# Performance work log

Measured on AMD Instinct MI355X. Metric: run time of the kernel, lower is better.

The kernel has to match this reference:

```python
import jax, jax.numpy as jnp
import numpy as np

N, C = 2, 256
GH0, GW0 = 40, 40
GH1, GW1 = 40, 40
STRIDE, TOPK = 2, 8
TEMP, THRESH, BORDER = 0.1, 0.2, 2
H0, W0 = GH0 * STRIDE, GW0 * STRIDE
H1, W1 = GH1 * STRIDE, GW1 * STRIDE
K4 = TOPK * STRIDE * STRIDE
# create_meshgrid(2,2) flattened: entries (x, y) in row-major (y outer) order
GRID = jnp.array([[0, 0], [1, 0], [0, 1], [1, 1]], dtype=jnp.int32)


def map_indices(idx, size0, size1):
    # idx: (n, G0, topk) coarse indices into image1 coarse grid
    row = idx[..., None] // size1[1] * STRIDE + GRID[:, 1]
    col = idx[..., None] % size1[1] * STRIDE + GRID[:, 0]
    fine = row * (size1[1] * STRIDE) + col  # (n, G0, topk, 4)
    n = idx.shape[0]
    fine = fine.reshape(n, size0[0], 1, size0[1], 1, -1)
    fine = jnp.broadcast_to(fine, (n, size0[0], STRIDE, size0[1], STRIDE, fine.shape[-1]))
    return fine.reshape(n, size0[0] * size0[1] * STRIDE * STRIDE, -1)


def remove_border_one_side(idx, br, size):
    h, w = size
    pos = jnp.arange(h * w)
    r, c = pos // w, pos % w
    border = (r < br) | (r >= h - br) | (c < br) | (c >= w - br)
    return jnp.where(border[None, :], 0, idx)


def unpatchify(x, grid, stride):
    n, g, s2, c = x.shape
    gh, gw = grid
    x = x.reshape(n, gh, gw, stride, stride, c)
    x = jnp.transpose(x, (0, 5, 1, 3, 2, 4))
    return x.reshape(n, c, gh * stride, gw * stride)


def fused_heatmaps(x0, x1, a01, a10, ind0_f, ind1_f):
    s01 = jnp.einsum('ngqc,ngkc->ngqk', x0, a01) / C  # (n, G0, 4, K4)
    s10 = jnp.einsum('ngqc,ngkc->ngqk', x1, a10) / C
    h01 = jax.nn.softmax(s01 / TEMP, axis=-1)
    h10 = jax.nn.softmax(s10 / TEMP, axis=-1)
    h01 = h01.reshape(N, GH0, GW0, STRIDE, STRIDE, K4)
    h01 = jnp.transpose(h01, (0, 1, 3, 2, 4, 5)).reshape(N, H0 * W0, K4)
    h10 = h10.reshape(N, GH1, GW1, STRIDE, STRIDE, K4)
    h10 = jnp.transpose(h10, (0, 5, 1, 3, 2, 4)).reshape(N, K4, H1 * W1)
    # dense scatter + gather mutual fusion (as in the torch code)
    b = jnp.arange(N)[:, None, None]
    l1 = jnp.arange(H1 * W1)[None, None, :]
    Z0 = jnp.zeros((N, H0 * W0, H1 * W1), h10.dtype).at[b, ind1_f, l1].set(h10)
    new_h01 = h01 * jnp.take_along_axis(Z0, ind0_f, axis=-1)
    l0 = jnp.arange(H0 * W0)[None, :, None]
    Z1 = jnp.zeros((N, H0 * W0, H1 * W1), h01.dtype).at[b, l0, ind0_f].set(h01)
    new_h10 = h10 * jnp.take_along_axis(Z1, ind1_f, axis=-2)
    return new_h01, new_h10


def coarse_matching(h01, h10, ind0_f, ind1_f):
    score = jnp.max(h01, axis=-1)                 # (n, L0)
    sub0 = jnp.argmax(h01, axis=-1)               # (n, L0)
    j_best = jnp.take_along_axis(ind0_f, sub0[..., None], axis=-1)[..., 0]
    sub1 = jnp.argmax(h10, axis=-2)               # (n, L1)
    i_best = jnp.take_along_axis(ind1_f, sub1[:, None, :], axis=-2)[:, 0, :]
    j_best = remove_border_one_side(j_best, BORDER, (H1, W1))
    i_best = remove_border_one_side(i_best, BORDER, (H0, W0))
    biproj = jnp.take_along_axis(i_best, j_best, axis=-1)
    mask = biproj == jnp.arange(H0 * W0)[None, :]
    mask = mask.at[:, 0].set(False)
    mask = mask & (score > THRESH)
    scores = jnp.where(mask, score, 0.0)
    return mask, j_best, scores


def setup_inputs() -> dict:
    key = jax.random.key(0)
    ks = jax.random.split(key, 6)
    return {
        'x0': jax.random.normal(ks[0], (N, GH0 * GW0, 4, C), jnp.float32),
        'x1': jax.random.normal(ks[1], (N, GH1 * GW1, 4, C), jnp.float32),
        'attended0_to_1': jax.random.normal(ks[2], (N, GH0 * GW0, K4, C), jnp.float32),
        'attended1_to_0': jax.random.normal(ks[3], (N, GH1 * GW1, K4, C), jnp.float32),
        'x0_prior': jax.random.normal(ks[4], (N, C, GH0, GW0), jnp.float32),
        'x1_prior': jax.random.normal(ks[5], (N, C, GH1, GW1), jnp.float32),
    }


def reference(x0, x1, attended0_to_1, attended1_to_0, x0_prior, x1_prior):
    p0 = x0_prior.reshape(N, C, GH0 * GW0)
    p1 = x1_prior.reshape(N, C, GH1 * GW1)
    sim = jnp.einsum('nci,ncj->nij', p0, p1) / C  # (n, G0, G1)
    _, i01 = jax.lax.top_k(sim, TOPK)                              # (n, G0, topk)
    _, i10 = jax.lax.top_k(jnp.swapaxes(sim, -2, -1), TOPK)        # (n, G1, topk)
    ind0_f = map_indices(i01, (GH0, GW0), (GH1, GW1))              # (n, L0, K4)
    ind1_f = jnp.swapaxes(map_indices(i10, (GH1, GW1), (GH0, GW0)), -2, -1)  # (n, K4, L1)
    h01, h10 = fused_heatmaps(x0, x1, attended0_to_1, attended1_to_0, ind0_f, ind1_f)
    mask, j_best, scores = coarse_matching(jax.lax.stop_gradient(h01), jax.lax.stop_gradient(h10), ind0_f, ind1_f)
    x0_8x = unpatchify(x0, (GH0, GW0), STRIDE)
    x1_8x = unpatchify(x1, (GH1, GW1), STRIDE)
    return h01, h10, scores, j_best, mask, x0_8x, x1_8x
```

## Files before the change

### kernel.cpp

```cpp
#include <hip/hip_runtime.h>


#define N_B   2
#define C_DIM 256
#define G0N   1600
#define GW    40
#define L0N   6400
#define W_F   80
#define TK    8

#define KC 32
#define HEAT_N   6400
#define SIM_BASE 6400
#define SIM_N    1250
#define UNP_BASE 7650
#define UNP_N    7680
#define MEGA_N   15330

__global__ __launch_bounds__(256) void k_mega(
    const float* __restrict__ x0,  const float* __restrict__ a01, float* __restrict__ h01p,
    const float* __restrict__ x1,  const float* __restrict__ a10, float* __restrict__ h10p,
    const float* __restrict__ p0,  const float* __restrict__ p1,
    float* __restrict__ sim, float* __restrict__ simT,
    float* __restrict__ out0, float* __restrict__ out1) {
  __shared__ __align__(16) float lds[4096];
  const int bid = blockIdx.x;
  const int t   = threadIdx.x;

  if (bid < HEAT_N) {
    const float* x   = x0;
    const float* att = a01;
    float*      hpre = h01p;
    int ng = bid;
    if (bid >= N_B * G0N) { x = x1; att = a10; hpre = h10p; ng = bid - N_B * G0N; }
    float* xs = lds;
    float (*dots)[33] = (float(*)[33])(lds + 1024);

    *(float4*)&xs[t * 4] = *(const float4*)(x + (size_t)ng * 4 * C_DIM + t * 4);

    const int row = t >> 3;
    const int sub = t & 7;
    const float* ar = att + ((size_t)ng * 32 + row) * C_DIM + sub * 4;
    float4 av[8];
#pragma unroll
    for (int it = 0; it < 8; ++it) av[it] = *(const float4*)(ar + it * 32);

    __syncthreads();

    float a0 = 0.f, a1 = 0.f, a2 = 0.f, a3 = 0.f;
#pragma unroll
    for (int it = 0; it < 8; ++it) {
      const int xo = sub * 4 + it * 32;
      float4 xv0 = *(const float4*)&xs[0 * C_DIM + xo];
      float4 xv1 = *(const float4*)&xs[1 * C_DIM + xo];
      float4 xv2 = *(const float4*)&xs[2 * C_DIM + xo];
      float4 xv3 = *(const float4*)&xs[3 * C_DIM + xo];
      a0 += av[it].x * xv0.x + av[it].y * xv0.y + av[it].z * xv0.z + av[it].w * xv0.w;
      a1 += av[it].x * xv1.x + av[it].y * xv1.y + av[it].z * xv1.z + av[it].w * xv1.w;
      a2 += av[it].x * xv2.x + av[it].y * xv2.y + av[it].z * xv2.z + av[it].w * xv2.w;
      a3 += av[it].x * xv3.x + av[it].y * xv3.y + av[it].z * xv3.z + av[it].w * xv3.w;
    }
#pragma unroll
    for (int off = 1; off < 8; off <<= 1) {
      a0 += __shfl_xor(a0, off);
      a1 += __shfl_xor(a1, off);
      a2 += __shfl_xor(a2, off);
      a3 += __shfl_xor(a3, off);
    }
    if (sub == 0) {
      dots[0][row] = a0;
      dots[1][row] = a1;
      dots[2][row] = a2;
      dots[3][row] = a3;
    }
    __syncthreads();
    if (t < 128) {
      int q = t >> 5, k4 = t & 31;
      float l = (dots[q][k4] * (1.0f / 256.0f)) / 0.1f;
      float m = l;
#pragma unroll
      for (int off = 1; off < 32; off <<= 1) m = fmaxf(m, __shfl_xor(m, off));
      float e = expf(l - m);
      float s = e;
#pragma unroll
      for (int off = 1; off < 32; off <<= 1) s += __shfl_xor(s, off);
      hpre[(size_t)ng * 128 + q * 32 + k4] = e / s;
    }
  } else if (bid < UNP_BASE) {
    int s = bid - SIM_BASE;
    const int n  = s / 625; s -= n * 625;
    const int i0 = (s / 25) * 64;
    const int j0 = (s % 25) * 64;
    const float* A = p0 + (size_t)n * C_DIM * G0N;
    const float* B = p1 + (size_t)n * C_DIM * G0N;
    float* As = lds;
    float* Bs = lds + 2048;
    const int tx = t & 15;
    const int ty = t >> 4;

    float4 acc[4];
#pragma unroll
    for (int ii = 0; ii < 4; ++ii) acc[ii] = make_float4(0.f, 0.f, 0.f, 0.f);

    for (int kc = 0; kc < C_DIM; kc += KC) {
#pragma unroll
      for (int u = 0; u < 2; ++u) {
        int f   = t + u * 256;
        int row = f >> 4;
        int c4  = (f & 15) * 4;
        *(float4*)&As[row * 64 + c4] = *(const float4*)(A + (size_t)(kc + row) * G0N + i0 + c4);
        *(float4*)&Bs[row * 64 + c4] = *(const float4*)(B + (size_t)(kc + row) * G0N + j0 + c4);
      }
      __syncthreads();
#pragma unroll
      for (int k = 0; k < KC; ++k) {
        __attribute__((aligned(16))) float a[4];
        *(float4*)&a[0] = *(const float4*)&As[k * 64 + ty * 4];
        float4 bv = *(const float4*)&Bs[k * 64 + tx * 4];
#pragma unroll
        for (int ii = 0; ii < 4; ++ii) {
          acc[ii].x += a[ii] * bv.x;
          acc[ii].y += a[ii] * bv.y;
          acc[ii].z += a[ii] * bv.z;
          acc[ii].w += a[ii] * bv.w;
        }
      }
      __syncthreads();
    }

    float* simn  = sim  + (size_t)n * G0N * G0N;
    float* simTn = simT + (size_t)n * G0N * G0N;
    const int ib = i0 + ty * 4;
    const int jb = j0 + tx * 4;
    const float* accf = (const float*)acc;
#pragma unroll
    for (int ii = 0; ii < 4; ++ii)
      *(float4*)(simn + (size_t)(ib + ii) * G0N + jb) = acc[ii];
#pragma unroll
    for (int jj = 0; jj < 4; ++jj) {
      float4 col = make_float4(accf[0 * 4 + jj], accf[1 * 4 + jj],
                               accf[2 * 4 + jj], accf[3 * 4 + jj]);
      *(float4*)(simTn + (size_t)(jb + jj) * G0N + ib) = col;
    }
  } else {
    int u = bid - UNP_BASE;
    int ux = u % 3; u /= 3;
    int r  = u % 80; u /= 80;
    int z  = u;
    const float* x = (z < 16) ? x0 : x1;
    float* out     = (z < 16) ? out0 : out1;
    int zz  = z & 15;
    int cc0 = ux * 32;
    int n   = zz >> 3;
    int c0  = (zz & 7) * 32;
    float (*tile)[33] = (float(*)[33])lds;
    int sr = r & 1, ghr = r >> 1;
    int pos = t >> 5, cl = t & 31;
#pragma unroll
    for (int it = 0; it < 4; ++it) {
      int p = pos + it * 8;
      int cc = cc0 + p;
      if (cc < W_F) {
        int gg = ghr * GW + (cc >> 1);
        int qq = (sr << 1) | (cc & 1);
        tile[p][cl] = x[(((size_t)n * G0N + gg) * 4 + qq) * C_DIM + c0 + cl];
      }
    }
    __syncthreads();
    int co = t >> 5, p2 = t & 31;
#pragma unroll
    for (int it = 0; it < 4; ++it) {
      int c = c0 + co + it * 8;
      int cc = cc0 + p2;
      if (cc < W_F)
        out[(((size_t)n * C_DIM + c) * W_F + r) * W_F + cc] = tile[p2][co + it * 8];
    }
  }
}

__global__ __launch_bounds__(256) void k_topk(const float* __restrict__ sim,
                                              const float* __restrict__ simT,
                                              int* __restrict__ i01,
                                              int* __restrict__ i10) {
  int wid  = (blockIdx.x * 256 + threadIdx.x) >> 6;
  int lane = threadIdx.x & 63;
  int dir  = wid / (N_B * G0N);
  int r    = wid - dir * (N_B * G0N);
  const float* row = (dir ? simT : sim) + (size_t)r * G0N;
  int* out = (dir ? i10 : i01) + r * TK;

  float v[25];
#pragma unroll
  for (int tt = 0; tt < 25; ++tt) v[tt] = row[lane + 64 * tt];

#pragma unroll 1
  for (int k = 0; k < TK; ++k) {
    float best = -3.4e38f; int bidx = 0x7fffffff;
#pragma unroll
    for (int tt = 0; tt < 25; ++tt) {
      if (v[tt] > best) { best = v[tt]; bidx = lane + 64 * tt; }
    }
#pragma unroll
    for (int off = 1; off < 64; off <<= 1) {
      float ov = __shfl_xor(best, off);
      int   oi = __shfl_xor(bidx, off);
      if (ov > best || (ov == best && oi < bidx)) { best = ov; bidx = oi; }
    }
    if (lane == 0) out[k] = bidx;
#pragma unroll
    for (int tt = 0; tt < 25; ++tt)
      if (lane + 64 * tt == bidx) v[tt] = -3.4e38f;
  }
}

__global__ __launch_bounds__(256) void k_fuse(const float* __restrict__ h01p,
                                              const float* __restrict__ h10p,
                                              const int* __restrict__ i01,
                                              const int* __restrict__ i10,
                                              float* __restrict__ h01_out,
                                              float* __restrict__ h10_out,
                                              float* __restrict__ score_ws,
                                              int* __restrict__ jbest_ws,
                                              float* __restrict__ jbest_out,
                                              int* __restrict__ ibest_ws) {
  if (blockIdx.x < 1600) {
    int idx = blockIdx.x * 8 + (threadIdx.x >> 5);
    int k4  = threadIdx.x & 31;
    int n = idx / L0N, l0 = idx - n * L0N;
    int r0 = l0 / W_F, c0 = l0 - r0 * W_F;
    int g0 = (r0 >> 1) * GW + (c0 >> 1);
    int q0 = ((r0 & 1) << 1) | (c0 & 1);
    int k = k4 >> 2, g = k4 & 3;
    int jc = i01[(n * G0N + g0) * TK + k];
    const int* row10 = i10 + (n * G0N + jc) * TK;
    int kf = -1;
#pragma unroll
    for (int kp = 0; kp < 8; ++kp) if (row10[kp] == g0) kf = kp;
    float m = 0.f;
    if (kf >= 0) m = h10p[((n * G0N + jc) * 4 + g) * 32 + kf * 4 + q0];
    float h = h01p[((n * G0N + g0) * 4 + q0) * 32 + k4];
    float val = h * m;
    h01_out[(size_t)idx * 32 + k4] = val;

    float best = val; int bi = k4;
#pragma unroll
    for (int off = 1; off < 32; off <<= 1) {
      float ov = __shfl_xor(best, off);
      int   oi = __shfl_xor(bi, off);
      if (ov > best || (ov == best && oi < bi)) { best = ov; bi = oi; }
    }
    if (k4 == 0) {
      score_ws[idx] = best;
      int kB = bi >> 2, gB = bi & 3;
      int jcB = i01[(n * G0N + g0) * TK + kB];
      int jrow = jcB / GW;
      int jb = ((jrow * 2 + (gB >> 1)) * W_F) + (jcB - jrow * GW) * 2 + (gB & 1);
      if (r0 < 2 || r0 >= W_F - 2 || c0 < 2 || c0 >= W_F - 2) jb = 0;
      jbest_ws[idx]  = jb;
      jbest_out[idx] = (float)jb;
    }
  } else {
    int idx = (blockIdx.x - 1600) * 8 + (threadIdx.x >> 5);
    int k4  = threadIdx.x & 31;
    int n = idx / L0N, l1 = idx - n * L0N;
    int r1 = l1 / W_F, c1 = l1 - r1 * W_F;
    int g1 = (r1 >> 1) * GW + (c1 >> 1);
    int q1 = ((r1 & 1) << 1) | (c1 & 1);
    int k = k4 >> 2, g = k4 & 3;
    int ic = i10[(n * G0N + g1) * TK + k];
    const int* row01 = i01 + (n * G0N + ic) * TK;
    int kf = -1;
#pragma unroll
    for (int kp = 0; kp < 8; ++kp) if (row01[kp] == g1) kf = kp;
    float m = 0.f;
    if (kf >= 0) m = h01p[((n * G0N + ic) * 4 + g) * 32 + kf * 4 + q1];
    float h = h10p[((n * G0N + g1) * 4 + q1) * 32 + k4];
    float val = h * m;
    h10_out[((size_t)n * 32 + k4) * L0N + l1] = val;

    float best = val; int bi = k4;
#pragma unroll
    for (int off = 1; off < 32; off <<= 1) {
      float ov = __shfl_xor(best, off);
      int   oi = __shfl_xor(bi, off);
      if (ov > best || (ov == best && oi < bi)) { best = ov; bi = oi; }
    }
    if (k4 == 0) {
      int kB = bi >> 2, gB = bi & 3;
      int icB = i10[(n * G0N + g1) * TK + kB];
      int irow = icB / GW;
      int ib = ((irow * 2 + (gB >> 1)) * W_F) + (icB - irow * GW) * 2 + (gB & 1);
      if (r1 < 2 || r1 >= W_F - 2 || c1 < 2 || c1 >= W_F - 2) ib = 0;
      ibest_ws[idx] = ib;
    }
  }
}

__global__ __launch_bounds__(256) void k_final(const float* __restrict__ score_ws,
                                               const int* __restrict__ jbest_ws,
                                               const int* __restrict__ ibest_ws,
                                               float* __restrict__ scores_out,
                                               float* __restrict__ mask_out) {
  int idx = blockIdx.x * 256 + threadIdx.x;
  if (idx >= N_B * L0N) return;
  int n = idx / L0N, l0 = idx - n * L0N;
  int jb = jbest_ws[idx];
  float sc = score_ws[idx];
  int biproj = ibest_ws[n * L0N + jb];
  bool mk = (biproj == l0) && (l0 != 0) && (sc > 0.2f);
  scores_out[idx] = mk ? sc : 0.f;
  mask_out[idx]   = mk ? 1.f : 0.f;
}

extern "C" void kernel_launch(void* const* d_in, const int* in_sizes, int n_in,
                              void* d_out, int out_size, void* d_ws, size_t ws_size,
                              hipStream_t stream) {
  const float* x0  = (const float*)d_in[0];
  const float* x1  = (const float*)d_in[1];
  const float* a01 = (const float*)d_in[2];
  const float* a10 = (const float*)d_in[3];
  const float* p0  = (const float*)d_in[4];
  const float* p1  = (const float*)d_in[5];
  float* out = (float*)d_out;

  float* ws       = (float*)d_ws;
  float* sim      = ws;
  float* simT     = ws + 5120000;
  int*   i01      = (int*)(ws + 10240000);
  int*   i10      = (int*)(ws + 10265600);
  float* h01p     = ws + 10291200;
  float* h10p     = ws + 10700800;
  float* score_ws = ws + 11110400;
  int*   jbest_ws = (int*)(ws + 11123200);
  int*   ibest_ws = (int*)(ws + 11136000);

  float* o_h01   = out;
  float* o_h10   = out + 409600;
  float* o_score = out + 819200;
  float* o_jbest = out + 832000;
  float* o_mask  = out + 844800;
  float* o_x08   = out + 857600;
  float* o_x18   = out + 4134400;

  k_mega<<<MEGA_N, 256, 0, stream>>>(x0, a01, h01p, x1, a10, h10p,
                                     p0, p1, sim, simT, o_x08, o_x18);
  k_topk<<<1600, 256, 0, stream>>>(sim, simT, i01, i10);
  k_fuse<<<3200, 256, 0, stream>>>(h01p, h10p, i01, i10, o_h01, o_h10,
                                   score_ws, jbest_ws, o_jbest, ibest_ws);
  k_final<<<50, 256, 0, stream>>>(score_ws, jbest_ws, ibest_ws, o_score, o_mask);
}
```

Before: 324.2 us.

## Batch four heatmap groups per block and interleave block roles across the grid

New measurement: 315.2 us. -2.8%, faster.

```diff
diff --git a/kernel.cpp b/kernel.cpp
--- a/kernel.cpp
+++ b/kernel.cpp
@@ -10,73 +10,94 @@
 #define TK    8
 
 #define KC 32
-#define HEAT_N   6400
-#define SIM_BASE 6400
-#define SIM_N    1250
-#define UNP_BASE 7650
-#define UNP_N    7680
-#define MEGA_N   15330
-
-__global__ __launch_bounds__(256) void k_mega(
+#define MEGA_N   10530
+
+__global__ __launch_bounds__(256, 4) void k_mega(
     const float* __restrict__ x0,  const float* __restrict__ a01, float* __restrict__ h01p,
     const float* __restrict__ x1,  const float* __restrict__ a10, float* __restrict__ h10p,
     const float* __restrict__ p0,  const float* __restrict__ p1,
     float* __restrict__ sim, float* __restrict__ simT,
     float* __restrict__ out0, float* __restrict__ out1) {
-  __shared__ __align__(16) float lds[4096];
+  __shared__ __align__(16) float lds[4624];
   const int bid = blockIdx.x;
   const int t   = threadIdx.x;
 
-  if (bid < HEAT_N) {
+  int hq = bid * 160;
+  bool is_heat = (hq % 1053) < 160;
+  int hid = hq / 1053;
+  int r2 = bid - (hq + 1052) / 1053;
+  int sq = r2 * 125;
+  bool is_sim = (sq % 893) < 125;
+  int sid = sq / 893;
+  int uid = r2 - (sq + 892) / 893;
+
+  if (is_heat) {
     const float* x   = x0;
     const float* att = a01;
     float*      hpre = h01p;
-    int ng = bid;
-    if (bid >= N_B * G0N) { x = x1; att = a10; hpre = h10p; ng = bid - N_B * G0N; }
-    float* xs = lds;
-    float (*dots)[33] = (float(*)[33])(lds + 1024);
-
-    *(float4*)&xs[t * 4] = *(const float4*)(x + (size_t)ng * 4 * C_DIM + t * 4);
+    int ng0 = hid * 4;
+    if (ng0 >= N_B * G0N) { x = x1; att = a10; hpre = h10p; ng0 -= N_B * G0N; }
 
     const int row = t >> 3;
     const int sub = t & 7;
-    const float* ar = att + ((size_t)ng * 32 + row) * C_DIM + sub * 4;
-    float4 av[8];
-#pragma unroll
-    for (int it = 0; it < 8; ++it) av[it] = *(const float4*)(ar + it * 32);
-
+    const float* arb = att + ((size_t)ng0 * 32 + row) * C_DIM + sub * 4;
+
+    float4 av[2][8];
+#pragma unroll
+    for (int it = 0; it < 8; ++it) av[0][it] = *(const float4*)(arb + it * 32);
+    const float* xb = x + (size_t)ng0 * 4 * C_DIM;
+#pragma unroll
+    for (int j = 0; j < 4; ++j) {
+      int f = t + j * 256;
+      *(float4*)&lds[f * 4] = *(const float4*)(xb + (size_t)f * 4);
+    }
+    float* dots = lds + 4096;
     __syncthreads();
 
-    float a0 = 0.f, a1 = 0.f, a2 = 0.f, a3 = 0.f;
-#pragma unroll
-    for (int it = 0; it < 8; ++it) {
-      const int xo = sub * 4 + it * 32;
-      float4 xv0 = *(const float4*)&xs[0 * C_DIM + xo];
-      float4 xv1 = *(const float4*)&xs[1 * C_DIM + xo];
-      float4 xv2 = *(const float4*)&xs[2 * C_DIM + xo];
-      float4 xv3 = *(const float4*)&xs[3 * C_DIM + xo];
-      a0 += av[it].x * xv0.x + av[it].y * xv0.y + av[it].z * xv0.z + av[it].w * xv0.w;
-      a1 += av[it].x * xv1.x + av[it].y * xv1.y + av[it].z * xv1.z + av[it].w * xv1.w;
-      a2 += av[it].x * xv2.x + av[it].y * xv2.y + av[it].z * xv2.z + av[it].w * xv2.w;
-      a3 += av[it].x * xv3.x + av[it].y * xv3.y + av[it].z * xv3.z + av[it].w * xv3.w;
-    }
-#pragma unroll
-    for (int off = 1; off < 8; off <<= 1) {
-      a0 += __shfl_xor(a0, off);
-      a1 += __shfl_xor(a1, off);
-      a2 += __shfl_xor(a2, off);
-      a3 += __shfl_xor(a3, off);
-    }
-    if (sub == 0) {
-      dots[0][row] = a0;
-      dots[1][row] = a1;
-      dots[2][row] = a2;
-      dots[3][row] = a3;
+#pragma unroll
+    for (int u = 0; u < 4; ++u) {
+      if (u < 3) {
+        const float* arn = arb + (size_t)(u + 1) * (32 * C_DIM);
+#pragma unroll
+        for (int it = 0; it < 8; ++it) av[(u + 1) & 1][it] = *(const float4*)(arn + it * 32);
+      }
+      __builtin_amdgcn_sched_barrier(0);
+      float a0 = 0.f, a1 = 0.f, a2 = 0.f, a3 = 0.f;
+#pragma unroll
+      for (int it = 0; it < 8; ++it) {
+        const float4 avv = av[u & 1][it];
+        const int xo = u * 1024 + sub * 4 + it * 32;
+        float4 xv0 = *(const float4*)&lds[xo + 0 * C_DIM];
+        float4 xv1 = *(const float4*)&lds[xo + 1 * C_DIM];
+        float4 xv2 = *(const float4*)&lds[xo + 2 * C_DIM];
+        float4 xv3 = *(const float4*)&lds[xo + 3 * C_DIM];
+        a0 += avv.x * xv0.x + avv.y * xv0.y + avv.z * xv0.z + avv.w * xv0.w;
+        a1 += avv.x * xv1.x + avv.y * xv1.y + avv.z * xv1.z + avv.w * xv1.w;
+        a2 += avv.x * xv2.x + avv.y * xv2.y + avv.z * xv2.z + avv.w * xv2.w;
+        a3 += avv.x * xv3.x + avv.y * xv3.y + avv.z * xv3.z + avv.w * xv3.w;
+      }
+#pragma unroll
+      for (int off = 1; off < 8; off <<= 1) {
+        a0 += __shfl_xor(a0, off);
+        a1 += __shfl_xor(a1, off);
+        a2 += __shfl_xor(a2, off);
+        a3 += __shfl_xor(a3, off);
+      }
+      if (sub == 0) {
+        dots[(u * 4 + 0) * 33 + row] = a0;
+        dots[(u * 4 + 1) * 33 + row] = a1;
+        dots[(u * 4 + 2) * 33 + row] = a2;
+        dots[(u * 4 + 3) * 33 + row] = a3;
+      }
     }
     __syncthreads();
-    if (t < 128) {
-      int q = t >> 5, k4 = t & 31;
-      float l = (dots[q][k4] * (1.0f / 256.0f)) / 0.1f;
+    const int lane32 = t & 31;
+    const int g0 = t >> 5;
+#pragma unroll
+    for (int p = 0; p < 2; ++p) {
+      int grp = g0 + p * 8;
+      int u = grp >> 2, q = grp & 3;
+      float l = (dots[grp * 33 + lane32] * (1.0f / 256.0f)) / 0.1f;
       float m = l;
 #pragma unroll
       for (int off = 1; off < 32; off <<= 1) m = fmaxf(m, __shfl_xor(m, off));
@@ -84,10 +105,10 @@
       float s = e;
 #pragma unroll
       for (int off = 1; off < 32; off <<= 1) s += __shfl_xor(s, off);
-      hpre[(size_t)ng * 128 + q * 32 + k4] = e / s;
-    }
-  } else if (bid < UNP_BASE) {
-    int s = bid - SIM_BASE;
+      hpre[(size_t)(ng0 + u) * 128 + q * 32 + lane32] = e / s;
+    }
+  } else if (is_sim) {
+    int s = sid;
     const int n  = s / 625; s -= n * 625;
     const int i0 = (s / 25) * 64;
     const int j0 = (s % 25) * 64;
@@ -106,10 +127,10 @@
 #pragma unroll
       for (int u = 0; u < 2; ++u) {
         int f   = t + u * 256;
-        int row = f >> 4;
+        int rw  = f >> 4;
         int c4  = (f & 15) * 4;
-        *(float4*)&As[row * 64 + c4] = *(const float4*)(A + (size_t)(kc + row) * G0N + i0 + c4);
-        *(float4*)&Bs[row * 64 + c4] = *(const float4*)(B + (size_t)(kc + row) * G0N + j0 + c4);
+        *(float4*)&As[rw * 64 + c4] = *(const float4*)(A + (size_t)(kc + rw) * G0N + i0 + c4);
+        *(float4*)&Bs[rw * 64 + c4] = *(const float4*)(B + (size_t)(kc + rw) * G0N + j0 + c4);
       }
       __syncthreads();
 #pragma unroll
@@ -143,7 +164,7 @@
       *(float4*)(simTn + (size_t)(jb + jj) * G0N + ib) = col;
     }
   } else {
-    int u = bid - UNP_BASE;
+    int u = uid;
     int ux = u % 3; u /= 3;
     int r  = u % 80; u /= 80;
     int z  = u;
```
